# Kernel tuning notes

Hardware: AMD Instinct MI355X
Metric: run time of the kernel (lower is better)

## Reference

```python
import jax, jax.numpy as jnp
import numpy as np

D_MODEL = 768
N_HEADS = 8
D_K = D_MODEL // N_HEADS
D_FF = 2048
EPS = 1e-5


def _layer_norm(x, gamma, beta):
    mu = jnp.mean(x, axis=-1, keepdims=True)
    var = jnp.mean(jnp.square(x - mu), axis=-1, keepdims=True)
    return (x - mu) * jax.lax.rsqrt(var + EPS) * gamma + beta


def setup_inputs() -> dict:
    key = jax.random.key(0)
    ks = jax.random.split(key, 16)
    s = 1.0 / np.sqrt(D_MODEL)
    sf = 1.0 / np.sqrt(D_FF)
    inp = {
        "x": jax.random.normal(ks[0], (4, 2048, D_MODEL), jnp.float32),
        "Wq": jax.random.uniform(ks[1], (D_MODEL, D_MODEL), jnp.float32, -s, s),
        "bq": jnp.zeros((D_MODEL,), jnp.float32),
        "Wk": jax.random.uniform(ks[2], (D_MODEL, D_MODEL), jnp.float32, -s, s),
        "bk": jnp.zeros((D_MODEL,), jnp.float32),
        "Wv": jax.random.uniform(ks[3], (D_MODEL, D_MODEL), jnp.float32, -s, s),
        "bv": jnp.zeros((D_MODEL,), jnp.float32),
        "Wo": jax.random.uniform(ks[4], (D_MODEL, D_MODEL), jnp.float32, -s, s),
        "bo": jnp.zeros((D_MODEL,), jnp.float32),
        "g1": jnp.ones((D_MODEL,), jnp.float32),
        "be1": jnp.zeros((D_MODEL,), jnp.float32),
        "W1": jax.random.uniform(ks[5], (D_MODEL, D_FF), jnp.float32, -s, s),
        "b1": jnp.zeros((D_FF,), jnp.float32),
        "W2": jax.random.uniform(ks[6], (D_FF, D_MODEL), jnp.float32, -sf, sf),
        "b2": jnp.zeros((D_MODEL,), jnp.float32),
        "g2": jnp.ones((D_MODEL,), jnp.float32),
        "be2": jnp.zeros((D_MODEL,), jnp.float32),
    }
    return inp


def reference(x, Wq, bq, Wk, bk, Wv, bv, Wo, bo, g1, be1, W1, b1, W2, b2, g2, be2):
    B, S, D = x.shape
    residual = x
    # projections, split into heads: [B, H, S, d_k]
    def proj(W, b):
        return (x @ W + b).reshape(B, S, N_HEADS, D_K).transpose(0, 2, 1, 3)
    Q, K, V = proj(Wq, bq), proj(Wk, bk), proj(Wv, bv)
    # explicit (non-fused) attention, as in the original
    scores = jnp.einsum('bhqd,bhkd->bhqk', Q, K) / np.sqrt(D_K)  # [B,H,S,S]
    attn = jax.nn.softmax(scores, axis=-1)
    out = jnp.einsum('bhqk,bhkd->bhqd', attn, V)
    out = out.transpose(0, 2, 1, 3).reshape(B, S, D)
    out = out @ Wo + bo
    x1 = _layer_norm(residual + out, g1, be1)
    ff = jax.nn.relu(x1 @ W1 + b1) @ W2 + b2
    return _layer_norm(x1 + ff, g2, be2)
```

## Files before the change

### kernel.cpp

```cpp
#include <hip/hip_runtime.h>
#include <cstdint>
#include <cstddef>

typedef unsigned short u16;
typedef __bf16 bf16x8 __attribute__((ext_vector_type(8)));
typedef float f32x4 __attribute__((ext_vector_type(4)));
typedef float f32x16 __attribute__((ext_vector_type(16)));

#define BATCH 4
#define SEQ   2048
#define DM    768
#define NH    8
#define DK    96
#define DFF   2048
#define MTOK  8192
#define QKVN  2304
#define LOG2E 1.44269504088896340736f

__device__ __forceinline__ u16 f2bf(float f) {
  union { float f; uint32_t u; } v; v.f = f;
  return (u16)((v.u + 0x7fffu + ((v.u >> 16) & 1u)) >> 16);
}
__device__ __forceinline__ float bf2f(u16 b) {
  union { uint32_t u; float f; } v; v.u = (uint32_t)b << 16;
  return v.f;
}
__device__ __forceinline__ bf16x8 ld8(const u16* p) { return *(const bf16x8*)p; }
__device__ __forceinline__ void async16(const u16* g, u16* l) {
  __builtin_amdgcn_global_load_lds((const __attribute__((address_space(1))) void*)g,
                                   (__attribute__((address_space(3))) void*)l, 16, 0, 0);
}

__global__ __launch_bounds__(256)
void prep(const float* __restrict__ x, u16* __restrict__ xb,
          const float* __restrict__ bq, const float* __restrict__ bk,
          const float* __restrict__ bv, float* __restrict__ bqkv,
          const float* __restrict__ Wq, const float* __restrict__ Wk,
          const float* __restrict__ Wv, const float* __restrict__ Wo,
          const float* __restrict__ W1, const float* __restrict__ W2,
          u16* __restrict__ WT, u16* __restrict__ WoT,
          u16* __restrict__ W1T, u16* __restrict__ W2T) {
  __shared__ float t[32][33];
  const int tid = threadIdx.x;
  int bid = blockIdx.x;

  if (bid < 6144) {
    size_t i = (size_t)bid * 1024 + tid * 4;
    float4 f = *(const float4*)(x + i);
    uint2 o;
    o.x = (unsigned)f2bf(f.x) | ((unsigned)f2bf(f.y) << 16);
    o.y = (unsigned)f2bf(f.z) | ((unsigned)f2bf(f.w) << 16);
    *(uint2*)(xb + i) = o;
    return;
  }
  if (bid < 6153) {
    int i = (bid - 6144) * 256 + tid;
    float v = (i < 768) ? bq[i] : (i < 1536) ? bk[i - 768] : bv[i - 1536];
    bqkv[i] = v;
    return;
  }
  bid -= 6153;
  const float* in; u16* out; int C, R, bx, by;
  if (bid < 576)       { in = Wq; out = WT;                 C = 768;  R = 768;  bx = bid % 24;          by = bid / 24; }
  else if (bid < 1152) { in = Wk; out = WT + 768 * 768;     C = 768;  R = 768;  bx = (bid - 576) % 24;  by = (bid - 576) / 24; }
  else if (bid < 1728) { in = Wv; out = WT + 2 * 768 * 768; C = 768;  R = 768;  bx = (bid - 1152) % 24; by = (bid - 1152) / 24; }
  else if (bid < 2304) { in = Wo; out = WoT;                C = 768;  R = 768;  bx = (bid - 1728) % 24; by = (bid - 1728) / 24; }
  else if (bid < 3840) { in = W1; out = W1T;                C = 2048; R = 768;  bx = (bid - 2304) % 64; by = (bid - 2304) / 64; }
  else                 { in = W2; out = W2T;                C = 768;  R = 2048; bx = (bid - 3840) % 24; by = (bid - 3840) / 24; }
  const int r0 = by * 32, c0 = bx * 32;
  const int tx = tid & 31, ty = tid >> 5;
#pragma unroll
  for (int i = 0; i < 4; i++)
    t[ty + i * 8][tx] = in[(size_t)(r0 + ty + i * 8) * C + c0 + tx];
  __syncthreads();
#pragma unroll
  for (int i = 0; i < 4; i++)
    out[(size_t)(c0 + ty + i * 8) * R + r0 + tx] = f2bf(t[tx][ty + i * 8]);
}

__global__ void transpose_v(const u16* __restrict__ v, u16* __restrict__ vt) {
  __shared__ u16 t[32][33];
  int bh = blockIdx.z, b = bh >> 3, h = bh & 7;
  int s0 = blockIdx.x * 32, d0 = blockIdx.y * 32;
  int tx = threadIdx.x, ty = threadIdx.y;
#pragma unroll
  for (int i = 0; i < 4; i++)
    t[ty + i * 8][tx] = v[(size_t)(b * SEQ + s0 + ty + i * 8) * QKVN + h * DK + d0 + tx];
  __syncthreads();
#pragma unroll
  for (int i = 0; i < 4; i++)
    vt[(size_t)(bh * DK + d0 + ty + i * 8) * SEQ + s0 + tx] = t[tx][ty + i * 8];
}

template <int RESID, int RELU, int OUTBF>
__global__ __launch_bounds__(256, 4)
void gemm_bt(const u16* __restrict__ A, const u16* __restrict__ BT,
             const float* __restrict__ bias, const float* __restrict__ resid,
             float* __restrict__ Cf, u16* __restrict__ Cb, int N, int K) {
  __shared__ __align__(16) u16 lA[128 * 64];
  __shared__ __align__(16) u16 lB[128 * 64];
  const int tid = threadIdx.x;
  const int wave = tid >> 6, lane = tid & 63;
  const int quad = lane >> 4, l16 = lane & 15;
  const int wm = wave >> 1, wn = wave & 1;
  const int tm = blockIdx.y * 128, tn = blockIdx.x * 128;

  f32x4 acc[4][4] = {};

  for (int k0 = 0; k0 < K; k0 += 64) {
    __syncthreads();
#pragma unroll
    for (int i = 0; i < 4; i++) {
      int cbase = (wave * 4 + i) * 64;
      int c = cbase + lane;
      int row = c >> 3;
      int scc = (c & 7) ^ (row & 7);
      async16(A + (size_t)(tm + row) * K + k0 + scc * 8, &lA[cbase * 8]);
      async16(BT + (size_t)(tn + row) * K + k0 + scc * 8, &lB[cbase * 8]);
    }
    __syncthreads();
#pragma unroll
    for (int ks = 0; ks < 2; ks++) {
      bf16x8 af[4], bfr[4];
#pragma unroll
      for (int i = 0; i < 4; i++) {
        int ra = wm * 64 + i * 16 + l16;
        af[i] = ld8(&lA[ra * 64 + (((ks * 4 + quad) ^ (ra & 7)) << 3)]);
        int rb = wn * 64 + i * 16 + l16;
        bfr[i] = ld8(&lB[rb * 64 + (((ks * 4 + quad) ^ (rb & 7)) << 3)]);
      }
#pragma unroll
      for (int i = 0; i < 4; i++)
#pragma unroll
        for (int j = 0; j < 4; j++)
          acc[i][j] = __builtin_amdgcn_mfma_f32_16x16x32_bf16(af[i], bfr[j], acc[i][j], 0, 0, 0);
    }
  }

#pragma unroll
  for (int i = 0; i < 4; i++) {
    const int row0 = tm + wm * 64 + i * 16 + quad * 4;
#pragma unroll
    for (int j = 0; j < 4; j++) {
      const int col = tn + wn * 64 + j * 16 + l16;
      const float bv = bias[col];
#pragma unroll
      for (int r = 0; r < 4; r++) {
        float v = acc[i][j][r] + bv;
        if (RESID) v += resid[(size_t)(row0 + r) * N + col];
        if (RELU) v = fmaxf(v, 0.f);
        if (OUTBF) Cb[(size_t)(row0 + r) * N + col] = f2bf(v);
        else       Cf[(size_t)(row0 + r) * N + col] = v;
      }
    }
  }
}

template <int RESID, int RELU, int OUTBF, int RESBF>
__global__ __launch_bounds__(256, 4)
void gemm_bt64(const u16* __restrict__ A, const u16* __restrict__ BT,
               const float* __restrict__ bias, const float* __restrict__ residf,
               const u16* __restrict__ residb,
               float* __restrict__ Cf, u16* __restrict__ Cb, int N, int K) {
  __shared__ __align__(16) u16 lA[128 * 64];
  __shared__ __align__(16) u16 lB[64 * 64];
  const int tid = threadIdx.x;
  const int wave = tid >> 6, lane = tid & 63;
  const int quad = lane >> 4, l16 = lane & 15;
  const int wm = wave >> 1, wn = wave & 1;
  const int tm = blockIdx.y * 128, tn = blockIdx.x * 64;

  f32x4 acc[4][2] = {};

  for (int k0 = 0; k0 < K; k0 += 64) {
    __syncthreads();
#pragma unroll
    for (int i = 0; i < 4; i++) {
      int cbase = (wave * 4 + i) * 64;
      int c = cbase + lane;
      int row = c >> 3;
      int scc = (c & 7) ^ (row & 7);
      async16(A + (size_t)(tm + row) * K + k0 + scc * 8, &lA[cbase * 8]);
    }
#pragma unroll
    for (int i = 0; i < 2; i++) {
      int cbase = (wave * 2 + i) * 64;
      int c = cbase + lane;
      int row = c >> 3;
      int scc = (c & 7) ^ (row & 7);
      async16(BT + (size_t)(tn + row) * K + k0 + scc * 8, &lB[cbase * 8]);
    }
    __syncthreads();
#pragma unroll
    for (int ks = 0; ks < 2; ks++) {
      bf16x8 af[4], bfr[2];
#pragma unroll
      for (int i = 0; i < 4; i++) {
        int ra = wm * 64 + i * 16 + l16;
        af[i] = ld8(&lA[ra * 64 + (((ks * 4 + quad) ^ (ra & 7)) << 3)]);
      }
#pragma unroll
      for (int j = 0; j < 2; j++) {
        int rb = wn * 32 + j * 16 + l16;
        bfr[j] = ld8(&lB[rb * 64 + (((ks * 4 + quad) ^ (rb & 7)) << 3)]);
      }
#pragma unroll
      for (int i = 0; i < 4; i++)
#pragma unroll
        for (int j = 0; j < 2; j++)
          acc[i][j] = __builtin_amdgcn_mfma_f32_16x16x32_bf16(af[i], bfr[j], acc[i][j], 0, 0, 0);
    }
  }

#pragma unroll
  for (int i = 0; i < 4; i++) {
    const int row0 = tm + wm * 64 + i * 16 + quad * 4;
#pragma unroll
    for (int j = 0; j < 2; j++) {
      const int col = tn + wn * 32 + j * 16 + l16;
      const float bv = bias[col];
#pragma unroll
      for (int r = 0; r < 4; r++) {
        float v = acc[i][j][r] + bv;
        if (RESID) {
          if (RESBF) v += bf2f(residb[(size_t)(row0 + r) * N + col]);
          else       v += residf[(size_t)(row0 + r) * N + col];
        }
        if (RELU) v = fmaxf(v, 0.f);
        if (OUTBF) Cb[(size_t)(row0 + r) * N + col] = f2bf(v);
        else       Cf[(size_t)(row0 + r) * N + col] = v;
      }
    }
  }
}

#define KROW 96
#define VROW 64

#define PACK_SLICE(SC, B, DST)                                                   \
  {                                                                              \
    uint32_t u0, u1, u2, u3;                                                     \
    asm("v_cvt_pk_bf16_f32 %0, %1, %2" : "=v"(u0) : "v"(SC[B+0]), "v"(SC[B+1])); \
    asm("v_cvt_pk_bf16_f32 %0, %1, %2" : "=v"(u1) : "v"(SC[B+2]), "v"(SC[B+3])); \
    asm("v_cvt_pk_bf16_f32 %0, %1, %2" : "=v"(u2) : "v"(SC[B+4]), "v"(SC[B+5])); \
    asm("v_cvt_pk_bf16_f32 %0, %1, %2" : "=v"(u3) : "v"(SC[B+6]), "v"(SC[B+7])); \
    asm("v_permlane32_swap_b32 %0, %1" : "+v"(u2), "+v"(u0));                    \
    asm("v_permlane32_swap_b32 %0, %1" : "+v"(u3), "+v"(u1));                    \
    union { uint32_t w[4]; bf16x8 v; } pu_;                                      \
    pu_.w[0] = u0; pu_.w[1] = u1; pu_.w[2] = u2; pu_.w[3] = u3;                  \
    DST = pu_.v;                                                                 \
  }

__global__ __launch_bounds__(512, 4)
void flash_attn(const u16* __restrict__ qkv, const u16* __restrict__ Vt,
                u16* __restrict__ Ob) {
  __shared__ __align__(16) u16 smem[24576];
  u16* lKp = smem;
  u16* lVp = smem + 12288;
  const int tid = threadIdx.x, wave = tid >> 6, lane = tid & 63;
  const int l32 = lane & 31, half = lane >> 5;
  const int qsub = wave >> 1, kodd = wave & 1, pair = wave >> 1;
  const int lin = blockIdx.x;
  const int bh = (lin & 7) * 4 + ((lin >> 3) & 3);
  const int qb = lin >> 5;
  const int b = bh >> 3, h = bh & 7;
  const int q0 = qb * 128 + qsub * 32;
  const u16* Qp = qkv;
  const u16* KpB = qkv + 768 + (size_t)b * SEQ * QKVN + h * DK;
  const u16* VtB = Vt + (size_t)bh * DK * SEQ;
  const float cs = 0.10206207262f * LOG2E;
  const float Ms = 16.0f * cs;

  bf16x8 qf[6];
#pragma unroll
  for (int d = 0; d < 6; d++)
    qf[d] = ld8(Qp + (size_t)(b * SEQ + q0 + l32) * QKVN + h * DK + d * 16 + half * 8);

  f32x16 of[3] = {};
  float l_lane = 0.f;

  auto stage = [&](int kt, int buf) {
    {
      int sl = tid;
      int row = sl / 12, s = sl % 12;
      int g = (s < 8) ? ((s ^ row) & 7) : (8 + ((s ^ row) & 3));
      async16(KpB + (size_t)(kt + row) * QKVN + g * 8, &lKp[buf * 6144 + sl * 8]);
    }
    if (tid < 256) {
      int sl = 512 + tid;
      int row = sl / 12, s = sl % 12;
      int g = (s < 8) ? ((s ^ row) & 7) : (8 + ((s ^ row) & 3));
      async16(KpB + (size_t)(kt + row) * QKVN + g * 8, &lKp[buf * 6144 + sl * 8]);
    }
    {
      int s = tid;
      int row = s >> 3, c = (s ^ row) & 7;
      async16(VtB + (size_t)row * SEQ + kt + c * 8, &lVp[buf * 6144 + s * 8]);
    }
    if (tid < 256) {
      int s = 512 + tid;
      int row = s >> 3, c = (s ^ row) & 7;
      async16(VtB + (size_t)row * SEQ + kt + c * 8, &lVp[buf * 6144 + s * 8]);
    }
  };

  stage(0, 0);
  int cur = 0;

  for (int kt = 0; kt < SEQ; kt += 64) {
    __syncthreads();
    if (kt + 64 < SEQ) stage(kt + 64, cur ^ 1);

    f32x16 sc = {};
    const int krow = kodd * 32 + l32;
    __builtin_amdgcn_s_setprio(1);
#pragma unroll
    for (int d = 0; d < 6; d++) {
      int g = d * 2 + half;
      int slot = (d < 4) ? ((g ^ krow) & 7) : (8 + ((g ^ krow) & 3));
      bf16x8 kb = ld8(&lKp[cur * 6144 + krow * KROW + slot * 8]);
      sc = __builtin_amdgcn_mfma_f32_32x32x16_bf16(kb, qf[d], sc, 0, 0, 0);
    }
    __builtin_amdgcn_s_setprio(0);

#pragma unroll
    for (int r = 0; r < 16; r++) {
      float p = __builtin_amdgcn_exp2f(sc[r] * cs - Ms);
      l_lane += p;
      sc[r] = p;
    }

    bf16x8 pa[2];
    PACK_SLICE(sc, 0, pa[0])
    PACK_SLICE(sc, 8, pa[1])

    __builtin_amdgcn_s_setprio(1);
#pragma unroll
    for (int ks = 0; ks < 2; ks++) {
      int gv = kodd * 4 + ks * 2 + half;
#pragma unroll
      for (int db = 0; db < 3; db++) {
        int vrow = db * 32 + l32;
        int slot = (gv ^ vrow) & 7;
        bf16x8 va = ld8(&lVp[cur * 6144 + vrow * VROW + slot * 8]);
        of[db] = __builtin_amdgcn_mfma_f32_32x32x16_bf16(va, pa[ks], of[db], 0, 0, 0);
      }
    }
    __builtin_amdgcn_s_setprio(0);
    cur ^= 1;
  }

  float lw = l_lane + __shfl_xor(l_lane, 32);
  float linv = 0.f;
  float* xf = (float*)smem;
  const int q = q0 + l32;
  u16* Orow = Ob + (size_t)(b * SEQ + q) * DM + h * DK;

  __syncthreads();
  if (kodd) {
    float* dst = xf + (pair * 64 + lane) * 33;
#pragma unroll
    for (int r = 0; r < 16; r++) { dst[r] = of[0][r]; dst[16 + r] = of[1][r]; }
    dst[32] = lw;
  }
  __syncthreads();
  if (!kodd) {
    const float* src = xf + (pair * 64 + lane) * 33;
    linv = 1.f / (lw + src[32]);
#pragma unroll
    for (int db = 0; db < 2; db++)
#pragma unroll
      for (int r = 0; r < 16; r++) {
        int dk = db * 32 + (r & 3) + 8 * (r >> 2) + 4 * half;
        Orow[dk] = f2bf((of[db][r] + src[db * 16 + r]) * linv);
      }
  }
  __syncthreads();
  if (kodd) {
    float* dst = xf + (pair * 64 + lane) * 16;
#pragma unroll
    for (int r = 0; r < 16; r++) dst[r] = of[2][r];
  }
  __syncthreads();
  if (!kodd) {
    const float* src = xf + (pair * 64 + lane) * 16;
#pragma unroll
    for (int r = 0; r < 16; r++) {
      int dk = 64 + (r & 3) + 8 * (r >> 2) + 4 * half;
      Orow[dk] = f2bf((of[2][r] + src[r]) * linv);
    }
  }
}

__global__ __launch_bounds__(256)
void ln_kernel(const float* __restrict__ y, const float* __restrict__ g,
               const float* __restrict__ be, float* __restrict__ outf,
               u16* __restrict__ outb) {
  int row = blockIdx.x, t = threadIdx.x;
  const float* yr = y + (size_t)row * DM;
  float v[3], s = 0.f, s2 = 0.f;
#pragma unroll
  for (int i = 0; i < 3; i++) {
    v[i] = yr[t + i * 256];
    s += v[i];
    s2 += v[i] * v[i];
  }
#pragma unroll
  for (int m = 1; m < 64; m <<= 1) {
    s += __shfl_xor(s, m);
    s2 += __shfl_xor(s2, m);
  }
  __shared__ float red[2][4];
  int w = t >> 6;
  if ((t & 63) == 0) { red[0][w] = s; red[1][w] = s2; }
  __syncthreads();
  s = red[0][0] + red[0][1] + red[0][2] + red[0][3];
  s2 = red[1][0] + red[1][1] + red[1][2] + red[1][3];
  float mu = s * (1.f / DM);
  float var = s2 * (1.f / DM) - mu * mu;
  float rs = rsqrtf(var + 1e-5f);
#pragma unroll
  for (int i = 0; i < 3; i++) {
    int e = t + i * 256;
    float o = (v[i] - mu) * rs * g[e] + be[e];
    if (outf) outf[(size_t)row * DM + e] = o;
    if (outb) outb[(size_t)row * DM + e] = f2bf(o);
  }
}

#define SZ_BF 12582912ull
#define SZ_F  25165824ull
#define O_XB   0ull
#define O_WT   (O_XB + SZ_BF)
#define O_WOT  (O_WT + 3538944ull)
#define O_W1T  (O_WOT + 1179648ull)
#define O_W2T  (O_W1T + 3145728ull)
#define O_QKV  (O_W2T + 3145728ull)
#define O_VT   (O_QKV + 37748736ull)
#define O_Y    (O_VT + SZ_BF)
#define O_X1F  (O_Y + SZ_F)
#define O_BIAS (O_X1F + SZ_F)

extern "C" void kernel_launch(void* const* d_in, const int* in_sizes, int n_in,
                              void* d_out, int out_size, void* d_ws, size_t ws_size,
                              hipStream_t stream) {
  const float* x   = (const float*)d_in[0];
  const float* Wq  = (const float*)d_in[1];
  const float* bq  = (const float*)d_in[2];
  const float* Wk  = (const float*)d_in[3];
  const float* bk  = (const float*)d_in[4];
  const float* Wv  = (const float*)d_in[5];
  const float* bv  = (const float*)d_in[6];
  const float* Wo  = (const float*)d_in[7];
  const float* bo  = (const float*)d_in[8];
  const float* g1  = (const float*)d_in[9];
  const float* be1 = (const float*)d_in[10];
  const float* W1  = (const float*)d_in[11];
  const float* b1  = (const float*)d_in[12];
  const float* W2  = (const float*)d_in[13];
  const float* b2  = (const float*)d_in[14];
  const float* g2  = (const float*)d_in[15];
  const float* be2 = (const float*)d_in[16];
  float* out = (float*)d_out;
  char* ws = (char*)d_ws;

  u16* xb    = (u16*)(ws + O_XB);
  u16* WT    = (u16*)(ws + O_WT);
  u16* WoT   = (u16*)(ws + O_WOT);
  u16* W1T   = (u16*)(ws + O_W1T);
  u16* W2T   = (u16*)(ws + O_W2T);
  u16* qkv   = (u16*)(ws + O_QKV);
  u16* vt    = (u16*)(ws + O_VT);
  float* y   = (float*)(ws + O_Y);
  float* bqkv = (float*)(ws + O_BIAS);
  u16* ao   = xb;
  u16* x1b  = qkv;
  u16* hbuf = qkv + (size_t)MTOK * DM;

  prep<<<11529, 256, 0, stream>>>(x, xb, bq, bk, bv, bqkv,
                                  Wq, Wk, Wv, Wo, W1, W2,
                                  WT, WoT, W1T, W2T);

  gemm_bt<0, 0, 1><<<dim3(18, 64), 256, 0, stream>>>(xb, WT, bqkv, nullptr, nullptr, qkv, QKVN, DM);
  transpose_v<<<dim3(64, 3, 32), dim3(32, 8), 0, stream>>>(qkv + 1536, vt);
  flash_attn<<<512, 512, 0, stream>>>(qkv, vt, ao);
  gemm_bt64<1, 0, 0, 0><<<dim3(12, 64), 256, 0, stream>>>(ao, WoT, bo, x, nullptr, y, nullptr, DM, DM);
  ln_kernel<<<8192, 256, 0, stream>>>(y, g1, be1, nullptr, x1b);
  gemm_bt<0, 1, 1><<<dim3(16, 64), 256, 0, stream>>>(x1b, W1T, b1, nullptr, nullptr, hbuf, DFF, DM);
  gemm_bt64<1, 0, 0, 1><<<dim3(12, 64), 256, 0, stream>>>(hbuf, W2T, b2, nullptr, x1b, y, nullptr, DM, DFF);
  ln_kernel<<<8192, 256, 0, stream>>>(y, g2, be2, out, nullptr);
}
```

Measured before the change: 342.8 us.

## Software-pipeline attention: overlap PV of previous tile with QK of current tile

Restructures the flash-attention loop so the P·V MFMAs for tile t-1 are issued right after the QK MFMAs for tile t, with the exp/pack of tile t done afterwards. This hides the softmax latency behind matrix work. V now uses a triple buffer so the previous tile's V stays valid while the next one is loaded. The K tile changes from an XOR-swizzled 96-element row to a padded 104-element row to avoid LDS bank conflicts. The cost is more LDS per block (about 62KB against 48KB before), which may lower occupancy under launch_bounds(512,4).

```diff
diff --git a/kernel.cpp b/kernel.cpp
--- a/kernel.cpp
+++ b/kernel.cpp
@@ -234,7 +234,7 @@
   }
 }
 
-#define KROW 96
+#define KROW 104
 #define VROW 64
 
 #define PACK_SLICE(SC, B, DST)                                                   \
@@ -254,9 +254,7 @@
 __global__ __launch_bounds__(512, 4)
 void flash_attn(const u16* __restrict__ qkv, const u16* __restrict__ Vt,
                 u16* __restrict__ Ob) {
-  __shared__ __align__(16) u16 smem[24576];
-  u16* lKp = smem;
-  u16* lVp = smem + 12288;
+  __shared__ __align__(16) u16 smem[31744];
   const int tid = threadIdx.x, wave = tid >> 6, lane = tid & 63;
   const int l32 = lane & 31, half = lane >> 5;
   const int qsub = wave >> 1, kodd = wave & 1, pair = wave >> 1;
@@ -278,48 +276,67 @@
 
   f32x16 of[3] = {};
   float l_lane = 0.f;
-
-  auto stage = [&](int kt, int buf) {
+  bf16x8 pa[2];
+
+  auto stage = [&](int kt, int kb_, int vb_) {
+    u16* kd = smem + kb_ * 6656;
+    u16* vd = smem + 13312 + vb_ * 6144;
     {
       int sl = tid;
-      int row = sl / 12, s = sl % 12;
-      int g = (s < 8) ? ((s ^ row) & 7) : (8 + ((s ^ row) & 3));
-      async16(KpB + (size_t)(kt + row) * QKVN + g * 8, &lKp[buf * 6144 + sl * 8]);
-    }
-    if (tid < 256) {
+      int row = sl / 13, s = sl - row * 13;
+      int c = s > 11 ? 11 : s;
+      async16(KpB + (size_t)(kt + row) * QKVN + c * 8, kd + sl * 8);
+    }
+    if (tid < 320) {
       int sl = 512 + tid;
-      int row = sl / 12, s = sl % 12;
-      int g = (s < 8) ? ((s ^ row) & 7) : (8 + ((s ^ row) & 3));
-      async16(KpB + (size_t)(kt + row) * QKVN + g * 8, &lKp[buf * 6144 + sl * 8]);
+      int row = sl / 13, s = sl - row * 13;
+      int c = s > 11 ? 11 : s;
+      async16(KpB + (size_t)(kt + row) * QKVN + c * 8, kd + sl * 8);
     }
     {
       int s = tid;
       int row = s >> 3, c = (s ^ row) & 7;
-      async16(VtB + (size_t)row * SEQ + kt + c * 8, &lVp[buf * 6144 + s * 8]);
+      async16(VtB + (size_t)row * SEQ + kt + c * 8, vd + s * 8);
     }
     if (tid < 256) {
       int s = 512 + tid;
       int row = s >> 3, c = (s ^ row) & 7;
-      async16(VtB + (size_t)row * SEQ + kt + c * 8, &lVp[buf * 6144 + s * 8]);
+      async16(VtB + (size_t)row * SEQ + kt + c * 8, vd + s * 8);
     }
   };
 
-  stage(0, 0);
-  int cur = 0;
-
-  for (int kt = 0; kt < SEQ; kt += 64) {
+  stage(0, 0, 0);
+  int vs = 1;
+  int vr = 0;
+  const int krow = kodd * 32 + l32;
+
+  for (int t = 0; t < 32; t++) {
     __syncthreads();
-    if (kt + 64 < SEQ) stage(kt + 64, cur ^ 1);
-
+    if (t + 1 < 32) stage((t + 1) * 64, (t + 1) & 1, vs);
+    vs = (vs == 2) ? 0 : vs + 1;
+
+    const u16* kd = smem + (t & 1) * 6656;
     f32x16 sc = {};
-    const int krow = kodd * 32 + l32;
     __builtin_amdgcn_s_setprio(1);
 #pragma unroll
     for (int d = 0; d < 6; d++) {
-      int g = d * 2 + half;
-      int slot = (d < 4) ? ((g ^ krow) & 7) : (8 + ((g ^ krow) & 3));
-      bf16x8 kb = ld8(&lKp[cur * 6144 + krow * KROW + slot * 8]);
+      bf16x8 kb = ld8(&kd[krow * KROW + (d * 2 + half) * 8]);
       sc = __builtin_amdgcn_mfma_f32_32x32x16_bf16(kb, qf[d], sc, 0, 0, 0);
+    }
+
+    if (t > 0) {
+      const u16* vd = smem + 13312 + vr * 6144;
+      vr = (vr == 2) ? 0 : vr + 1;
+#pragma unroll
+      for (int ks = 0; ks < 2; ks++) {
+        int gv = kodd * 4 + ks * 2 + half;
+#pragma unroll
+        for (int db = 0; db < 3; db++) {
+          int vrow = db * 32 + l32;
+          bf16x8 va = ld8(&vd[vrow * VROW + ((gv ^ vrow) & 7) * 8]);
+          of[db] = __builtin_amdgcn_mfma_f32_32x32x16_bf16(va, pa[ks], of[db], 0, 0, 0);
+        }
+      }
     }
     __builtin_amdgcn_s_setprio(0);
 
@@ -329,25 +346,22 @@
       l_lane += p;
       sc[r] = p;
     }
-
-    bf16x8 pa[2];
     PACK_SLICE(sc, 0, pa[0])
     PACK_SLICE(sc, 8, pa[1])
-
-    __builtin_amdgcn_s_setprio(1);
+  }
+
+  {
+    const u16* vd = smem + 13312 + vr * 6144;
 #pragma unroll
     for (int ks = 0; ks < 2; ks++) {
       int gv = kodd * 4 + ks * 2 + half;
 #pragma unroll
       for (int db = 0; db < 3; db++) {
         int vrow = db * 32 + l32;
-        int slot = (gv ^ vrow) & 7;
-        bf16x8 va = ld8(&lVp[cur * 6144 + vrow * VROW + slot * 8]);
+        bf16x8 va = ld8(&vd[vrow * VROW + ((gv ^ vrow) & 7) * 8]);
         of[db] = __builtin_amdgcn_mfma_f32_32x32x16_bf16(va, pa[ks], of[db], 0, 0, 0);
       }
     }
-    __builtin_amdgcn_s_setprio(0);
-    cur ^= 1;
   }
 
   float lw = l_lane + __shfl_xor(l_lane, 32);
```

New measurement: 340.7 us. No clear change (-0.6%).
